# Performance work log

Measured on AMD Instinct MI355X. Metric: run time of the kernel, lower is better.

Reference implementation:

```python
import jax, jax.numpy as jnp
import numpy as np

NEG_BIG = -9e15

def setup_inputs() -> dict:
    key = jax.random.key(0)
    k1, k2, k3, k4 = jax.random.split(key, 4)
    N, Fin, Fout = 8192, 128, 64
    x = jax.random.normal(k1, (N, Fin), dtype=jnp.float32)
    adj = jax.random.randint(k2, (N, N), 0, 2).astype(jnp.float32)
    W = jax.random.normal(k3, (Fin, Fout), dtype=jnp.float32) * (1.0 / np.sqrt(Fin))
    a = jax.random.normal(k4, (2 * Fout, 1), dtype=jnp.float32) * (1.0 / np.sqrt(2 * Fout))
    return {"x": x, "adj": adj, "W": W, "a": a}

def reference(x, adj, W, a):
    Fout = W.shape[1]
    Wh = x @ W                              # [N, Fout]
    Wh1 = Wh @ a[:Fout, :]                  # [N, 1]
    Wh2 = Wh @ a[Fout:, :]                  # [N, 1]
    e = jax.nn.leaky_relu(Wh1 + Wh2.T, negative_slope=0.2)  # [N, N]
    attention = jnp.where(adj > 0, e, NEG_BIG)
    attention = jax.nn.softmax(attention, axis=1)
    # dropout is identity in eval mode (training=False)
    h_prime = attention @ Wh                # [N, Fout]
    return jax.nn.elu(h_prime)
```

## Files before the change

kernel.cpp:

```cpp
#include <hip/hip_runtime.h>
#include <cstdint>
#include <cstddef>


#define NN   8192
#define FIN  128
#define FOUT 64
#define SJ   16
#define JCHUNK (NN / SJ)

typedef __attribute__((ext_vector_type(8))) short   short8;
typedef __attribute__((ext_vector_type(4))) float   f32x4;

#define LOG2E 1.44269504088896340736f
#define NTL(p) __builtin_nontemporal_load((const f32x4*)(p))

__global__ __launch_bounds__(256) void gat_phaseA(
    const float* __restrict__ x, const float* __restrict__ W,
    const float* __restrict__ a, unsigned short* __restrict__ Whbt,
    float* __restrict__ Wh1, float* __restrict__ Wh2)
{
  const int wid  = threadIdx.x >> 6;
  const int lane = threadIdx.x & 63;
  const int row0 = (blockIdx.x * 4 + wid) * 4;
  const float a1 = a[lane];
  const float a2 = a[FOUT + lane];
  float acc[4] = {0.f, 0.f, 0.f, 0.f};
#pragma unroll 4
  for (int k = 0; k < FIN; k += 4) {
    float4 wv0 = make_float4(W[(k+0)*FOUT + lane], W[(k+1)*FOUT + lane],
                             W[(k+2)*FOUT + lane], W[(k+3)*FOUT + lane]);
#pragma unroll
    for (int r = 0; r < 4; ++r) {
      float4 xv = *(const float4*)(x + (row0 + r) * FIN + k);
      acc[r] = fmaf(xv.x, wv0.x, acc[r]);
      acc[r] = fmaf(xv.y, wv0.y, acc[r]);
      acc[r] = fmaf(xv.z, wv0.z, acc[r]);
      acc[r] = fmaf(xv.w, wv0.w, acc[r]);
    }
  }
#pragma unroll
  for (int r = 0; r < 4; ++r) {
    unsigned int u = __float_as_uint(acc[r]);
    unsigned int rb = (u + 0x7FFFu + ((u >> 16) & 1u)) >> 16;
    Whbt[lane * NN + row0 + r] = (unsigned short)rb;
    float s1 = acc[r] * a1, s2 = acc[r] * a2;
#pragma unroll
    for (int off = 32; off; off >>= 1) {
      s1 += __shfl_xor(s1, off);
      s2 += __shfl_xor(s2, off);
    }
    if (lane == 0) { Wh1[row0 + r] = s1 * LOG2E; Wh2[row0 + r] = s2 * LOG2E; }
  }
}

#define AF_ONE(AF, AD0, AD1, W20, W21, WH1, RS)                          \
    _Pragma("unroll")                                                    \
    for (int e = 0; e < 4; ++e) {                                        \
      float t0 = (WH1) + (W20)[e];                                       \
      t0 = fmaxf(t0, 0.2f * t0);              \
      float p0 = exp2f(t0) * (AD0)[e];         \
      unsigned int pu0 = __float_as_uint(p0) & 0xFFFF0000u;              \
      RS += __uint_as_float(pu0);            \
      AF[e] = (short)(pu0 >> 16);                                        \
      float t1 = (WH1) + (W21)[e];                                       \
      t1 = fmaxf(t1, 0.2f * t1);                                         \
      float p1 = exp2f(t1) * (AD1)[e];                                   \
      unsigned int pu1 = __float_as_uint(p1) & 0xFFFF0000u;              \
      RS += __uint_as_float(pu1);                                        \
      AF[4 + e] = (short)(pu1 >> 16);                                    \
    }

#define GAT_BODY(AD00, AD01, AD10, AD11, W2C0, W2C1, BC0, BC1, BC2, BC3, \
                 W2N0, W2N1, BN0, BN1, BN2, BN3, JN1, JN2)               \
  {                                                                      \
    W2N0 = *(const f32x4*)(w2base + (JN1));                              \
    W2N1 = *(const f32x4*)(w2base + (JN1) + 4);                          \
    BN0  = *(const short8*)(bbase + (JN1));                              \
    BN1  = *(const short8*)(bbase + (JN1) + 16 * NN);                    \
    BN2  = *(const short8*)(bbase + (JN1) + 32 * NN);                    \
    BN3  = *(const short8*)(bbase + (JN1) + 48 * NN);                    \
    short8 af0, af1;                                                     \
    AF_ONE(af0, AD00, AD01, W2C0, W2C1, wh1_0, rsum0);                   \
    AF_ONE(af1, AD10, AD11, W2C0, W2C1, wh1_1, rsum1);                   \
    AD00 = NTL(adjrow0 + (JN2)); AD01 = NTL(adjrow0 + (JN2) + 4);        \
    AD10 = NTL(adjrow1 + (JN2)); AD11 = NTL(adjrow1 + (JN2) + 4);        \
    c00 = __builtin_amdgcn_mfma_f32_16x16x32_bf16(af0, BC0, c00, 0,0,0); \
    c01 = __builtin_amdgcn_mfma_f32_16x16x32_bf16(af0, BC1, c01, 0,0,0); \
    c02 = __builtin_amdgcn_mfma_f32_16x16x32_bf16(af0, BC2, c02, 0,0,0); \
    c03 = __builtin_amdgcn_mfma_f32_16x16x32_bf16(af0, BC3, c03, 0,0,0); \
    c10 = __builtin_amdgcn_mfma_f32_16x16x32_bf16(af1, BC0, c10, 0,0,0); \
    c11 = __builtin_amdgcn_mfma_f32_16x16x32_bf16(af1, BC1, c11, 0,0,0); \
    c12 = __builtin_amdgcn_mfma_f32_16x16x32_bf16(af1, BC2, c12, 0,0,0); \
    c13 = __builtin_amdgcn_mfma_f32_16x16x32_bf16(af1, BC3, c13, 0,0,0); \
  }

__global__ __launch_bounds__(256, 3) void gat_phaseB(
    const float* __restrict__ adj, const unsigned short* __restrict__ Whbt,
    const float* __restrict__ Wh1, const float* __restrict__ Wh2,
    float* __restrict__ accbuf, float* __restrict__ denbuf, int nslices)
{
  const int wid  = threadIdx.x >> 6;
  const int lane = threadIdx.x & 63;
  const int jc   = blockIdx.x % SJ;
  const int rg   = (blockIdx.x / SJ) * 4 + wid;
  const int m = lane & 15;
  const int q = lane >> 4;
  const int r0 = rg * 32 + m;
  const int r1 = r0 + 16;
  const float wh1_0 = Wh1[r0];
  const float wh1_1 = Wh1[r1];
  const float* adjrow0 = adj + (size_t)r0 * NN + q * 8;
  const float* adjrow1 = adj + (size_t)r1 * NN + q * 8;
  const unsigned short* bbase = Whbt + m * NN + q * 8;
  const float* w2base = Wh2 + q * 8;

  f32x4 c00 = {0.f,0.f,0.f,0.f}, c01 = c00, c02 = c00, c03 = c00;
  f32x4 c10 = c00, c11 = c00, c12 = c00, c13 = c00;
  float rsum0 = 0.f, rsum1 = 0.f;

  const int jbeg = jc * JCHUNK;

  f32x4 w2A0, w2A1, w2B0, w2B1;
  short8 bA0, bA1, bA2, bA3, bB0, bB1, bB2, bB3;
  f32x4 adA00, adA01, adA10, adA11;
  f32x4 adB00, adB01, adB10, adB11;

  w2A0 = *(const f32x4*)(w2base + jbeg);
  w2A1 = *(const f32x4*)(w2base + jbeg + 4);
  bA0  = *(const short8*)(bbase + jbeg);
  bA1  = *(const short8*)(bbase + jbeg + 16 * NN);
  bA2  = *(const short8*)(bbase + jbeg + 32 * NN);
  bA3  = *(const short8*)(bbase + jbeg + 48 * NN);
  adA00 = NTL(adjrow0 + jbeg);      adA01 = NTL(adjrow0 + jbeg + 4);
  adA10 = NTL(adjrow1 + jbeg);      adA11 = NTL(adjrow1 + jbeg + 4);
  adB00 = NTL(adjrow0 + jbeg + 32); adB01 = NTL(adjrow0 + jbeg + 36);
  adB10 = NTL(adjrow1 + jbeg + 32); adB11 = NTL(adjrow1 + jbeg + 36);

#pragma unroll
  for (int bb = 0; bb < 16; bb += 2) {
    const int j1 = (bb + 1 < 16) ? (bb + 1) * 32 : 0;
    const int j2 = (bb + 2 < 16) ? (bb + 2) * 32 : 0;
    const int j3 = (bb + 3 < 16) ? (bb + 3) * 32 : 0;
    GAT_BODY(adA00, adA01, adA10, adA11, w2A0, w2A1, bA0, bA1, bA2, bA3,
             w2B0, w2B1, bB0, bB1, bB2, bB3, jbeg + j1, jbeg + j2);
    GAT_BODY(adB00, adB01, adB10, adB11, w2B0, w2B1, bB0, bB1, bB2, bB3,
             w2A0, w2A1, bA0, bA1, bA2, bA3, jbeg + j2, jbeg + j3);
  }

  rsum0 += __shfl_xor(rsum0, 16);
  rsum0 += __shfl_xor(rsum0, 32);
  rsum1 += __shfl_xor(rsum1, 16);
  rsum1 += __shfl_xor(rsum1, 32);

  const int slice = (nslices > 1) ? jc : 0;
  float* accout = accbuf + (size_t)slice * (NN * FOUT);
  float* denout = denbuf + slice * NN;
  f32x4 cc0[4] = {c00, c01, c02, c03};
  f32x4 cc1[4] = {c10, c11, c12, c13};
  if (nslices > 1) {
    if (q == 0) { denout[r0] = rsum0; denout[r1] = rsum1; }
#pragma unroll
    for (int ft = 0; ft < 4; ++ft)
#pragma unroll
      for (int r = 0; r < 4; ++r) {
        accout[(rg * 32 +      q * 4 + r) * FOUT + ft * 16 + m] = cc0[ft][r];
        accout[(rg * 32 + 16 + q * 4 + r) * FOUT + ft * 16 + m] = cc1[ft][r];
      }
  } else {
    if (q == 0) { atomicAdd(&denout[r0], rsum0); atomicAdd(&denout[r1], rsum1); }
#pragma unroll
    for (int ft = 0; ft < 4; ++ft)
#pragma unroll
      for (int r = 0; r < 4; ++r) {
        atomicAdd(&accout[(rg * 32 +      q * 4 + r) * FOUT + ft * 16 + m], cc0[ft][r]);
        atomicAdd(&accout[(rg * 32 + 16 + q * 4 + r) * FOUT + ft * 16 + m], cc1[ft][r]);
      }
  }
}

__global__ __launch_bounds__(256) void gat_phaseC(
    const float* __restrict__ accbuf, const float* __restrict__ denbuf,
    float* __restrict__ out, int nslices)
{
  const int idx4 = blockIdx.x * 256 + threadIdx.x;
  const int idx  = idx4 * 4;
  const int row  = idx >> 6;
  f32x4 s = {0.f, 0.f, 0.f, 0.f};
  float d = 0.f;
  for (int sl = 0; sl < nslices; ++sl) {
    f32x4 v = *(const f32x4*)(accbuf + (size_t)sl * (NN * FOUT) + idx);
    s += v;
    d += denbuf[sl * NN + row];
  }
  float inv = 1.0f / d;
  f32x4 o;
#pragma unroll
  for (int e = 0; e < 4; ++e) {
    float v = s[e] * inv;
    o[e] = (v > 0.f) ? v : expm1f(v);
  }
  *(f32x4*)(out + idx) = o;
}

extern "C" void kernel_launch(void* const* d_in, const int* in_sizes, int n_in,
                              void* d_out, int out_size, void* d_ws, size_t ws_size,
                              hipStream_t stream)
{
  const float* x   = (const float*)d_in[0];
  const float* adj = (const float*)d_in[1];
  const float* W   = (const float*)d_in[2];
  const float* a   = (const float*)d_in[3];
  float* out = (float*)d_out;

  const size_t accEl = (size_t)NN * FOUT;
  const size_t roomyBytes = (size_t)SJ * accEl * 4 + (size_t)SJ * NN * 4
                          + (size_t)NN * 8 + (size_t)FOUT * NN * 2;
  const int nslices = (ws_size >= roomyBytes) ? SJ : 1;

  char* ws = (char*)d_ws;
  float* accbuf = (float*)ws;
  size_t off = (size_t)nslices * accEl * 4;
  float* denbuf = (float*)(ws + off); off += (size_t)nslices * NN * 4;
  float* Wh1 = (float*)(ws + off);    off += (size_t)NN * 4;
  float* Wh2 = (float*)(ws + off);    off += (size_t)NN * 4;
  unsigned short* Whbt = (unsigned short*)(ws + off);

  if (nslices == 1)
    hipMemsetAsync(accbuf, 0, accEl * 4 + (size_t)NN * 4, stream);

  gat_phaseA<<<NN / 16, 256, 0, stream>>>(x, W, a, Whbt, Wh1, Wh2);
  gat_phaseB<<<((NN / 32) * SJ) / 4, 256, 0, stream>>>(adj, Whbt, Wh1, Wh2,
                                                       accbuf, denbuf, nslices);
  gat_phaseC<<<(NN * FOUT) / 4 / 256, 256, 0, stream>>>(accbuf, denbuf, out, nslices);
}
```

Before: 393.4 us.

## Pack adjacency into bitmask in a separate pass, feed phaseB from bits

```diff
diff --git a/kernel.cpp b/kernel.cpp
--- a/kernel.cpp
+++ b/kernel.cpp
@@ -11,9 +11,33 @@
 
 typedef __attribute__((ext_vector_type(8))) short   short8;
 typedef __attribute__((ext_vector_type(4))) float   f32x4;
+typedef __attribute__((ext_vector_type(4))) unsigned int u32x4;
 
 #define LOG2E 1.44269504088896340736f
-#define NTL(p) __builtin_nontemporal_load((const f32x4*)(p))
+
+__global__ __launch_bounds__(256) void gat_mask(
+    const float* __restrict__ adj, unsigned char* __restrict__ maskb)
+{
+  const int wid  = threadIdx.x >> 6;
+  const int lane = threadIdx.x & 63;
+  const int row  = blockIdx.x;
+  const float* ar = adj + (size_t)row * NN;
+  unsigned char* mr = maskb + (size_t)row * (NN / 8);
+#pragma unroll
+  for (int k = 0; k < 4; ++k) {
+    const int c = wid + 4 * k;
+    const float* p = ar + c * 512 + lane * 8;
+    f32x4 v0 = *(const f32x4*)(p);
+    f32x4 v1 = *(const f32x4*)(p + 4);
+    unsigned int byte = 0;
+#pragma unroll
+    for (int e = 0; e < 4; ++e) {
+      byte |= (v0[e] > 0.f) ? (1u << e)       : 0u;
+      byte |= (v1[e] > 0.f) ? (1u << (4 + e)) : 0u;
+    }
+    mr[c * 64 + (lane & 3) * 16 + (lane >> 2)] = (unsigned char)byte;
+  }
+}
 
 __global__ __launch_bounds__(256) void gat_phaseA(
     const float* __restrict__ x, const float* __restrict__ W,
@@ -54,25 +78,25 @@
   }
 }
 
-#define AF_ONE(AF, AD0, AD1, W20, W21, WH1, RS)                          \
+#define AF_ONE(AF, BYTE, W20, W21, WH1, RS)                              \
     _Pragma("unroll")                                                    \
     for (int e = 0; e < 4; ++e) {                                        \
       float t0 = (WH1) + (W20)[e];                                       \
       t0 = fmaxf(t0, 0.2f * t0);              \
-      float p0 = exp2f(t0) * (AD0)[e];         \
+      float p0 = ((BYTE) & (1u << e)) ? exp2f(t0) : 0.0f;                \
       unsigned int pu0 = __float_as_uint(p0) & 0xFFFF0000u;              \
       RS += __uint_as_float(pu0);            \
       AF[e] = (short)(pu0 >> 16);                                        \
       float t1 = (WH1) + (W21)[e];                                       \
       t1 = fmaxf(t1, 0.2f * t1);                                         \
-      float p1 = exp2f(t1) * (AD1)[e];                                   \
+      float p1 = ((BYTE) & (1u << (4 + e))) ? exp2f(t1) : 0.0f;          \
       unsigned int pu1 = __float_as_uint(p1) & 0xFFFF0000u;              \
       RS += __uint_as_float(pu1);                                        \
       AF[4 + e] = (short)(pu1 >> 16);                                    \
     }
 
-#define GAT_BODY(AD00, AD01, AD10, AD11, W2C0, W2C1, BC0, BC1, BC2, BC3, \
-                 W2N0, W2N1, BN0, BN1, BN2, BN3, JN1, JN2)               \
+#define GAT_BODY(T, W2C0, W2C1, BC0, BC1, BC2, BC3,                      \
+                 W2N0, W2N1, BN0, BN1, BN2, BN3, JN1)                    \
   {                                                                      \
     W2N0 = *(const f32x4*)(w2base + (JN1));                              \
     W2N1 = *(const f32x4*)(w2base + (JN1) + 4);                          \
@@ -80,11 +104,11 @@
     BN1  = *(const short8*)(bbase + (JN1) + 16 * NN);                    \
     BN2  = *(const short8*)(bbase + (JN1) + 32 * NN);                    \
     BN3  = *(const short8*)(bbase + (JN1) + 48 * NN);                    \
+    const unsigned int by0 = (mk0[(T) >> 2] >> (((T) & 3) * 8)) & 0xffu; \
+    const unsigned int by1 = (mk1[(T) >> 2] >> (((T) & 3) * 8)) & 0xffu; \
     short8 af0, af1;                                                     \
-    AF_ONE(af0, AD00, AD01, W2C0, W2C1, wh1_0, rsum0);                   \
-    AF_ONE(af1, AD10, AD11, W2C0, W2C1, wh1_1, rsum1);                   \
-    AD00 = NTL(adjrow0 + (JN2)); AD01 = NTL(adjrow0 + (JN2) + 4);        \
-    AD10 = NTL(adjrow1 + (JN2)); AD11 = NTL(adjrow1 + (JN2) + 4);        \
+    AF_ONE(af0, by0, W2C0, W2C1, wh1_0, rsum0);                          \
+    AF_ONE(af1, by1, W2C0, W2C1, wh1_1, rsum1);                          \
     c00 = __builtin_amdgcn_mfma_f32_16x16x32_bf16(af0, BC0, c00, 0,0,0); \
     c01 = __builtin_amdgcn_mfma_f32_16x16x32_bf16(af0, BC1, c01, 0,0,0); \
     c02 = __builtin_amdgcn_mfma_f32_16x16x32_bf16(af0, BC2, c02, 0,0,0); \
@@ -95,8 +119,8 @@
     c13 = __builtin_amdgcn_mfma_f32_16x16x32_bf16(af1, BC3, c13, 0,0,0); \
   }
 
-__global__ __launch_bounds__(256, 3) void gat_phaseB(
-    const float* __restrict__ adj, const unsigned short* __restrict__ Whbt,
+__global__ __launch_bounds__(256, 4) void gat_phaseB(
+    const unsigned char* __restrict__ maskb, const unsigned short* __restrict__ Whbt,
     const float* __restrict__ Wh1, const float* __restrict__ Wh2,
     float* __restrict__ accbuf, float* __restrict__ denbuf, int nslices)
 {
@@ -110,10 +134,11 @@
   const int r1 = r0 + 16;
   const float wh1_0 = Wh1[r0];
   const float wh1_1 = Wh1[r1];
-  const float* adjrow0 = adj + (size_t)r0 * NN + q * 8;
-  const float* adjrow1 = adj + (size_t)r1 * NN + q * 8;
   const unsigned short* bbase = Whbt + m * NN + q * 8;
   const float* w2base = Wh2 + q * 8;
+
+  const u32x4 mk0 = *(const u32x4*)(maskb + (size_t)r0 * (NN/8) + jc * 64 + q * 16);
+  const u32x4 mk1 = *(const u32x4*)(maskb + (size_t)r1 * (NN/8) + jc * 64 + q * 16);
 
   f32x4 c00 = {0.f,0.f,0.f,0.f}, c01 = c00, c02 = c00, c03 = c00;
   f32x4 c10 = c00, c11 = c00, c12 = c00, c13 = c00;
@@ -123,8 +148,6 @@
 
   f32x4 w2A0, w2A1, w2B0, w2B1;
   short8 bA0, bA1, bA2, bA3, bB0, bB1, bB2, bB3;
-  f32x4 adA00, adA01, adA10, adA11;
-  f32x4 adB00, adB01, adB10, adB11;
 
   w2A0 = *(const f32x4*)(w2base + jbeg);
   w2A1 = *(const f32x4*)(w2base + jbeg + 4);
@@ -132,20 +155,15 @@
   bA1  = *(const short8*)(bbase + jbeg + 16 * NN);
   bA2  = *(const short8*)(bbase + jbeg + 32 * NN);
   bA3  = *(const short8*)(bbase + jbeg + 48 * NN);
-  adA00 = NTL(adjrow0 + jbeg);      adA01 = NTL(adjrow0 + jbeg + 4);
-  adA10 = NTL(adjrow1 + jbeg);      adA11 = NTL(adjrow1 + jbeg + 4);
-  adB00 = NTL(adjrow0 + jbeg + 32); adB01 = NTL(adjrow0 + jbeg + 36);
-  adB10 = NTL(adjrow1 + jbeg + 32); adB11 = NTL(adjrow1 + jbeg + 36);
 
 #pragma unroll
   for (int bb = 0; bb < 16; bb += 2) {
     const int j1 = (bb + 1 < 16) ? (bb + 1) * 32 : 0;
     const int j2 = (bb + 2 < 16) ? (bb + 2) * 32 : 0;
-    const int j3 = (bb + 3 < 16) ? (bb + 3) * 32 : 0;
-    GAT_BODY(adA00, adA01, adA10, adA11, w2A0, w2A1, bA0, bA1, bA2, bA3,
-             w2B0, w2B1, bB0, bB1, bB2, bB3, jbeg + j1, jbeg + j2);
-    GAT_BODY(adB00, adB01, adB10, adB11, w2B0, w2B1, bB0, bB1, bB2, bB3,
-             w2A0, w2A1, bA0, bA1, bA2, bA3, jbeg + j2, jbeg + j3);
+    GAT_BODY(bb,     w2A0, w2A1, bA0, bA1, bA2, bA3,
+             w2B0, w2B1, bB0, bB1, bB2, bB3, jbeg + j1);
+    GAT_BODY(bb + 1, w2B0, w2B1, bB0, bB1, bB2, bB3,
+             w2A0, w2A1, bA0, bA1, bA2, bA3, jbeg + j2);
   }
 
   rsum0 += __shfl_xor(rsum0, 16);
@@ -214,8 +232,9 @@
   float* out = (float*)d_out;
 
   const size_t accEl = (size_t)NN * FOUT;
+  const size_t maskBytes = (size_t)NN * (NN / 8);
   const size_t roomyBytes = (size_t)SJ * accEl * 4 + (size_t)SJ * NN * 4
-                          + (size_t)NN * 8 + (size_t)FOUT * NN * 2;
+                          + (size_t)NN * 8 + (size_t)FOUT * NN * 2 + maskBytes;
   const int nslices = (ws_size >= roomyBytes) ? SJ : 1;
 
   char* ws = (char*)d_ws;
@@ -224,13 +243,15 @@
   float* denbuf = (float*)(ws + off); off += (size_t)nslices * NN * 4;
   float* Wh1 = (float*)(ws + off);    off += (size_t)NN * 4;
   float* Wh2 = (float*)(ws + off);    off += (size_t)NN * 4;
-  unsigned short* Whbt = (unsigned short*)(ws + off);
+  unsigned short* Whbt = (unsigned short*)(ws + off); off += (size_t)FOUT * NN * 2;
+  unsigned char* maskb = (unsigned char*)(ws + off);
 
   if (nslices == 1)
     hipMemsetAsync(accbuf, 0, accEl * 4 + (size_t)NN * 4, stream);
 
+  gat_mask<<<NN, 256, 0, stream>>>(adj, maskb);
   gat_phaseA<<<NN / 16, 256, 0, stream>>>(x, W, a, Whbt, Wh1, Wh2);
-  gat_phaseB<<<((NN / 32) * SJ) / 4, 256, 0, stream>>>(adj, Whbt, Wh1, Wh2,
+  gat_phaseB<<<((NN / 32) * SJ) / 4, 256, 0, stream>>>(maskb, Whbt, Wh1, Wh2,
                                                        accbuf, denbuf, nslices);
   gat_phaseC<<<(NN * FOUT) / 4 / 256, 256, 0, stream>>>(accbuf, denbuf, out, nslices);
 }
```

New measurement: 426.9 us. 8.5% more time.
